# Kernel optimization log

Measured on AMD Instinct MI355X. Metric: run time of the kernel, lower is better.

Reference implementation:

```python
import jax, jax.numpy as jnp
import numpy as np
import math

B, S, H, N = 64, 512, 768, 16
C_COMP, C_REL = 5, 3
P = N * (N - 1)
LN_EPS = 1e-5

# ordered pair indices (i, j), i != j, row-major like the torch double loop
_PAIR_I, _PAIR_J = np.nonzero(~np.eye(N, dtype=bool))
_PAIR_I = jnp.asarray(_PAIR_I)
_PAIR_J = jnp.asarray(_PAIR_J)


def setup_inputs() -> dict:
    key = jax.random.key(0)
    ks = jax.random.split(key, 20)
    sc = 0.02
    p = lambda k, shape: (jax.random.normal(k, shape, jnp.float32) * sc)
    return {
        "last_hidden_state": jax.random.normal(ks[0], (B, S, H), jnp.float32),
        "span_starts": jax.random.randint(ks[1], (B, N), 0, 480).astype(jnp.int32),
        "span_lengths": jax.random.randint(ks[2], (B, N), 0, 31).astype(jnp.int32),
        "components": jax.random.randint(ks[3], (B, N), 0, C_COMP).astype(jnp.int32),
        "relations": jax.random.randint(ks[4], (B, P), 0, C_REL).astype(jnp.int32),
        # comp_classifier: Linear(H,512) -> Tanh -> Linear(512,C_COMP)
        "comp_w1": p(ks[5], (H, 512)), "comp_b1": jnp.zeros((512,), jnp.float32),
        "comp_w2": p(ks[6], (512, C_COMP)), "comp_b2": jnp.zeros((C_COMP,), jnp.float32),
        # Attention(H, H), no bias
        "wq": p(ks[7], (H, H)), "wk": p(ks[8], (H, H)), "wv": p(ks[9], (H, H)),
        # LayerNorm(H)
        "ln_g": jnp.ones((H,), jnp.float32), "ln_b": jnp.zeros((H,), jnp.float32),
        # rel_classifier: Linear(2H,512) -> Tanh -> Linear(512,C_REL)
        "rel_w1": p(ks[10], (2 * H, 512)), "rel_b1": jnp.zeros((512,), jnp.float32),
        "rel_w2": p(ks[11], (512, C_REL)), "rel_b2": jnp.zeros((C_REL,), jnp.float32),
    }


def _ce_mean(logits, gold):
    # logits [M, C], gold [M] -> scalar mean cross entropy
    logp = jax.nn.log_softmax(logits, axis=-1)
    return -jnp.mean(jnp.take_along_axis(logp, gold[:, None].astype(jnp.int32), axis=-1))


def reference(last_hidden_state, span_starts, span_lengths, components, relations,
              comp_w1, comp_b1, comp_w2, comp_b2,
              wq, wk, wv, ln_g, ln_b,
              rel_w1, rel_b1, rel_w2, rel_b2):
    # --- per-span mean pooling (inclusive end = start + length), masked+vectorized ---
    pos = jnp.arange(S)
    ends = span_starts + span_lengths
    mask = ((pos[None, None, :] >= span_starts[:, :, None]) &
            (pos[None, None, :] <= ends[:, :, None])).astype(jnp.float32)  # [B,N,S]
    lens = (span_lengths + 1).astype(jnp.float32)
    pooled = jnp.einsum('bns,bsh->bnh', mask, last_hidden_state) / lens[:, :, None]  # [B,N,H]
    # dropout(p=0.2) is identity in eval mode

    # --- component classifier ---
    comp_logits = jnp.tanh(pooled @ comp_w1 + comp_b1) @ comp_w2 + comp_b2  # [B,N,C_COMP]

    # --- small self-attention over spans ---
    q = pooled @ wq; k = pooled @ wk; v = pooled @ wv
    scores = jax.nn.softmax(jnp.einsum('bnd,bmd->bnm', q, k) / math.sqrt(H), axis=-1)
    attn = jnp.einsum('bnm,bmh->bnh', scores, v)

    # --- residual + layernorm ---
    x = pooled + attn
    mu = jnp.mean(x, axis=-1, keepdims=True)
    var = jnp.mean((x - mu) ** 2, axis=-1, keepdims=True)
    x = (x - mu) * jax.lax.rsqrt(var + LN_EPS) * ln_g + ln_b  # [B,N,H]

    # --- O(N^2) pairwise relation classification (ordered pairs i != j) ---
    pair_feat = jnp.concatenate([x[:, _PAIR_I, :], x[:, _PAIR_J, :]], axis=-1)  # [B,P,2H]
    rel_logits = jnp.tanh(pair_feat @ rel_w1 + rel_b1) @ rel_w2 + rel_b2  # [B,P,C_REL]

    loss_comp = _ce_mean(comp_logits.reshape(-1, C_COMP), components.reshape(-1))
    loss_rel = _ce_mean(rel_logits.reshape(-1, C_REL), relations.reshape(-1))
    return (comp_logits.reshape(-1, C_COMP), rel_logits.reshape(-1, C_REL), loss_comp, loss_rel)
```

## Files before the change

### kernel.cpp

```cpp
#include <hip/hip_runtime.h>

#define BB 64
#define SS 512
#define HH 768
#define NSPAN 16
#define PP 240
#define CCOMP 5
#define CREL 3

typedef unsigned short u16;
typedef __attribute__((ext_vector_type(8))) short bf16x8;
typedef __attribute__((ext_vector_type(4))) float f32x4;

__device__ __forceinline__ u16 f2bf(float f) {
    union { float f; unsigned int i; } v; v.f = f;
    unsigned int x = v.i;
    unsigned int lsb = (x >> 16) & 1u;
    x += 0x7fffu + lsb;
    return (u16)(x >> 16);
}

__device__ __forceinline__ float ftanh(float x) {
    float xc = fminf(fmaxf(x, -15.f), 15.f);
    float e = __expf(2.f * xc);
    return (e - 1.f) / (e + 1.f);
}

__global__ __launch_bounds__(256) void prep_kernel(
    const float* __restrict__ cw1, const float* __restrict__ wq,
    const float* __restrict__ wk, const float* __restrict__ wv,
    const float* __restrict__ rw1, u16* __restrict__ wcat_t, u16* __restrict__ relw_t) {
    int blk = blockIdx.x;
    const float* W; int ldw, nt; u16* outp;
    if (blk < 384)        {             W = cw1; ldw = 512; nt = 16; outp = wcat_t; }
    else if (blk < 960)   { blk -= 384; W = wq;  ldw = 768; nt = 24; outp = wcat_t + (size_t)512 * 768; }
    else if (blk < 1536)  { blk -= 960; W = wk;  ldw = 768; nt = 24; outp = wcat_t + (size_t)1280 * 768; }
    else if (blk < 2112)  { blk -= 1536; W = wv; ldw = 768; nt = 24; outp = wcat_t + (size_t)2048 * 768; }
    else if (blk < 2496)  { blk -= 2112; W = rw1; ldw = 512; nt = 16; outp = relw_t; }
    else                  { blk -= 2496; W = rw1 + (size_t)768 * 512; ldw = 512; nt = 16; outp = relw_t + (size_t)512 * 768; }
    int tk = blk / nt, tn = blk % nt;
    int k0 = tk * 32, n0 = tn * 32;
    __shared__ u16 Ls[32][36];
    int tid = threadIdx.x;
    int tx = tid & 31, ty = tid >> 5;
#pragma unroll
    for (int r = 0; r < 4; ++r) {
        int k = ty + r * 8;
        Ls[tx][k] = f2bf(W[(size_t)(k0 + k) * ldw + n0 + tx]);
    }
    __syncthreads();
#pragma unroll
    for (int r = 0; r < 4; ++r) {
        int n = ty + r * 8;
        outp[(size_t)(n0 + n) * 768 + k0 + tx] = Ls[n][tx];
    }
}

__global__ __launch_bounds__(256) void pool_kernel(
    const float* __restrict__ lhs, const int* __restrict__ starts,
    const int* __restrict__ lens, float* __restrict__ pooled, u16* __restrict__ pooled_bf) {
    int bn = blockIdx.x;
    int b = bn >> 4;
    int st = starts[bn];
    int ln = lens[bn];
    int tid = threadIdx.x;
    const float* base = lhs + ((size_t)b * SS + st) * HH;
    float a0 = 0.f, a1 = 0.f, a2 = 0.f;
    for (int s = 0; s <= ln; ++s) {
        const float* row = base + (size_t)s * HH;
        a0 += row[tid];
        a1 += row[tid + 256];
        a2 += row[tid + 512];
    }
    float inv = 1.0f / (float)(ln + 1);
    a0 *= inv; a1 *= inv; a2 *= inv;
    float* out = pooled + (size_t)bn * HH;
    u16* outb = pooled_bf + (size_t)bn * HH;
    out[tid] = a0;       out[tid + 256] = a1;       out[tid + 512] = a2;
    outb[tid] = f2bf(a0); outb[tid + 256] = f2bf(a1); outb[tid + 512] = f2bf(a2);
}

__global__ __launch_bounds__(256) void gemm_pw_kernel(
    const u16* __restrict__ pooled_bf, const u16* __restrict__ wcat_t,
    const float* __restrict__ comp_b1, float* __restrict__ y2) {
    __shared__ u16 As[64][72];
    __shared__ u16 Bs[64][72];
    int ccol0 = blockIdx.x * 64;
    int row0 = blockIdx.y * 64;
    int act = (ccol0 < 512);
    int tid = threadIdx.x;
    int lane = tid & 63, w = tid >> 6;
    int q = lane >> 4, l15 = lane & 15;
    int wm = (w & 1) * 32, wn = (w >> 1) * 32;
    int r = tid >> 2, c0 = (tid & 3) * 16;
    const u16* ga = pooled_bf + (size_t)(row0 + r) * 768 + c0;
    const u16* gb = wcat_t + (size_t)(ccol0 + r) * 768 + c0;
    f32x4 acc[2][2];
#pragma unroll
    for (int i = 0; i < 2; ++i)
#pragma unroll
        for (int j = 0; j < 2; ++j) acc[i][j] = (f32x4){0.f, 0.f, 0.f, 0.f};

    uint4 va0 = *(const uint4*)(ga);
    uint4 va1 = *(const uint4*)(ga + 8);
    uint4 vb0 = *(const uint4*)(gb);
    uint4 vb1 = *(const uint4*)(gb + 8);
    for (int k0 = 0; k0 < 768; k0 += 64) {
        __syncthreads();
        *(uint4*)(&As[r][c0]) = va0;
        *(uint4*)(&As[r][c0 + 8]) = va1;
        *(uint4*)(&Bs[r][c0]) = vb0;
        *(uint4*)(&Bs[r][c0 + 8]) = vb1;
        __syncthreads();
        if (k0 + 64 < 768) {
            va0 = *(const uint4*)(ga + k0 + 64);
            va1 = *(const uint4*)(ga + k0 + 72);
            vb0 = *(const uint4*)(gb + k0 + 64);
            vb1 = *(const uint4*)(gb + k0 + 72);
        }
#pragma unroll
        for (int ks = 0; ks < 2; ++ks) {
            bf16x8 a0 = *(const bf16x8*)(&As[wm + l15][ks * 32 + q * 8]);
            bf16x8 a1 = *(const bf16x8*)(&As[wm + 16 + l15][ks * 32 + q * 8]);
            bf16x8 b0 = *(const bf16x8*)(&Bs[wn + l15][ks * 32 + q * 8]);
            bf16x8 b1 = *(const bf16x8*)(&Bs[wn + 16 + l15][ks * 32 + q * 8]);
            acc[0][0] = __builtin_amdgcn_mfma_f32_16x16x32_bf16(a0, b0, acc[0][0], 0, 0, 0);
            acc[0][1] = __builtin_amdgcn_mfma_f32_16x16x32_bf16(a0, b1, acc[0][1], 0, 0, 0);
            acc[1][0] = __builtin_amdgcn_mfma_f32_16x16x32_bf16(a1, b0, acc[1][0], 0, 0, 0);
            acc[1][1] = __builtin_amdgcn_mfma_f32_16x16x32_bf16(a1, b1, acc[1][1], 0, 0, 0);
        }
    }
#pragma unroll
    for (int tm = 0; tm < 2; ++tm)
#pragma unroll
        for (int tn = 0; tn < 2; ++tn)
#pragma unroll
            for (int reg = 0; reg < 4; ++reg) {
                int rr = row0 + wm + tm * 16 + q * 4 + reg;
                int cc = ccol0 + wn + tn * 16 + l15;
                float v = acc[tm][tn][reg];
                if (act) v = ftanh(v + comp_b1[cc]);
                y2[(size_t)rr * 2816 + cc] = v;
            }
}

__global__ __launch_bounds__(256) void gemm_z_kernel(
    const u16* __restrict__ x_bf, const u16* __restrict__ relw_t, float* __restrict__ Z) {
    __shared__ u16 As[32][72];
    __shared__ u16 Bs[64][72];
    int ccol0 = blockIdx.x * 64;
    int row0 = blockIdx.y * 32;
    int tid = threadIdx.x;
    int lane = tid & 63, w = tid >> 6;
    int q = lane >> 4, l15 = lane & 15;
    int wm = (w & 1) * 16, wn = (w >> 1) * 32;
    int ra = tid >> 3, ca = (tid & 7) * 8;
    int rb = tid >> 2, cb = (tid & 3) * 16;
    const u16* ga = x_bf + (size_t)(row0 + ra) * 768 + ca;
    const u16* gb = relw_t + (size_t)(ccol0 + rb) * 768 + cb;
    f32x4 acc[2];
    acc[0] = (f32x4){0.f, 0.f, 0.f, 0.f};
    acc[1] = (f32x4){0.f, 0.f, 0.f, 0.f};

    uint4 va = *(const uint4*)(ga);
    uint4 vb0 = *(const uint4*)(gb);
    uint4 vb1 = *(const uint4*)(gb + 8);
    for (int k0 = 0; k0 < 768; k0 += 64) {
        __syncthreads();
        *(uint4*)(&As[ra][ca]) = va;
        *(uint4*)(&Bs[rb][cb]) = vb0;
        *(uint4*)(&Bs[rb][cb + 8]) = vb1;
        __syncthreads();
        if (k0 + 64 < 768) {
            va = *(const uint4*)(ga + k0 + 64);
            vb0 = *(const uint4*)(gb + k0 + 64);
            vb1 = *(const uint4*)(gb + k0 + 72);
        }
#pragma unroll
        for (int ks = 0; ks < 2; ++ks) {
            bf16x8 a0 = *(const bf16x8*)(&As[wm + l15][ks * 32 + q * 8]);
            bf16x8 b0 = *(const bf16x8*)(&Bs[wn + l15][ks * 32 + q * 8]);
            bf16x8 b1 = *(const bf16x8*)(&Bs[wn + 16 + l15][ks * 32 + q * 8]);
            acc[0] = __builtin_amdgcn_mfma_f32_16x16x32_bf16(a0, b0, acc[0], 0, 0, 0);
            acc[1] = __builtin_amdgcn_mfma_f32_16x16x32_bf16(a0, b1, acc[1], 0, 0, 0);
        }
    }
#pragma unroll
    for (int tn = 0; tn < 2; ++tn)
#pragma unroll
        for (int reg = 0; reg < 4; ++reg) {
            int rr = row0 + wm + q * 4 + reg;
            int cc = ccol0 + wn + tn * 16 + l15;
            Z[(size_t)rr * 1024 + cc] = acc[tn][reg];
        }
}

__global__ __launch_bounds__(256) void attn_ln_kernel(
    const float* __restrict__ y2, const float* __restrict__ pooled,
    const float* __restrict__ ln_g, const float* __restrict__ ln_b,
    u16* __restrict__ x_bf) {
    __shared__ float ks[16][772];
    __shared__ float Ssm[16][17];
    int b = blockIdx.x;
    int tid = threadIdx.x;
    int n = tid >> 4;
    int hl = tid & 15;

    for (int u = 0; u < 48; ++u) {
        int h = hl + (u << 4);
        ks[n][h] = y2[((size_t)(b * 16 + n)) * 2816 + 1280 + h];
    }
    __syncthreads();

    int m = tid & 15;
    const float* qrow = y2 + ((size_t)(b * 16 + n)) * 2816 + 512;
    float dot = 0.f;
    for (int h = 0; h < 768; h += 4) {
        float4 qv = *(const float4*)(qrow + h);
        float4 kv = *(const float4*)(&ks[m][h]);
        dot += qv.x * kv.x + qv.y * kv.y + qv.z * kv.z + qv.w * kv.w;
    }
    float sval = dot * 0.03608439182435161f;
    float mx = sval;
#pragma unroll
    for (int off = 8; off >= 1; off >>= 1) mx = fmaxf(mx, __shfl_xor(mx, off, 16));
    float pexp = __expf(sval - mx);
    float psum = pexp;
#pragma unroll
    for (int off = 8; off >= 1; off >>= 1) psum += __shfl_xor(psum, off, 16);
    Ssm[n][m] = pexp / psum;
    __syncthreads();

    for (int u = 0; u < 48; ++u) {
        int h = hl + (u << 4);
        ks[n][h] = y2[((size_t)(b * 16 + n)) * 2816 + 2048 + h];
    }
    __syncthreads();

    float sc[16];
#pragma unroll
    for (int mm = 0; mm < 16; ++mm) sc[mm] = Ssm[n][mm];
    int row = b * 16 + n;
    const float* prow = pooled + (size_t)row * HH;
    float xv[48];
    float ssum = 0.f, ssq = 0.f;
    for (int u = 0; u < 48; ++u) {
        int h = hl + (u << 4);
        float a = 0.f;
#pragma unroll
        for (int mm = 0; mm < 16; ++mm) a += sc[mm] * ks[mm][h];
        float v = prow[h] + a;
        xv[u] = v;
        ssum += v;
        ssq += v * v;
    }
#pragma unroll
    for (int off = 8; off >= 1; off >>= 1) {
        ssum += __shfl_xor(ssum, off, 16);
        ssq += __shfl_xor(ssq, off, 16);
    }
    float mu = ssum * (1.0f / 768.0f);
    float var = ssq * (1.0f / 768.0f) - mu * mu;
    float rs = rsqrtf(var + 1e-5f);
    u16* xrow_bf = x_bf + (size_t)row * HH;
    for (int u = 0; u < 48; ++u) {
        int h = hl + (u << 4);
        xrow_bf[h] = f2bf((xv[u] - mu) * rs * ln_g[h] + ln_b[h]);
    }
}

__global__ __launch_bounds__(256) void heads_kernel(
    const float* __restrict__ Z, const float* __restrict__ rb1,
    const float* __restrict__ rw2, const float* __restrict__ rb2,
    const int* __restrict__ rels,
    const float* __restrict__ y2, const float* __restrict__ cw2,
    const float* __restrict__ cb2, const int* __restrict__ comps,
    float* __restrict__ out, float* __restrict__ rel_p, float* __restrict__ comp_p) {
    __shared__ float red[4];
    int wave = threadIdx.x >> 6, lane = threadIdx.x & 63;
    if (blockIdx.x < 3840) {
        int row = blockIdx.x * 4 + wave;
        int b = row / PP;
        int p = row - b * PP;
        int i = p / 15;
        int jj = p - i * 15;
        int j = jj + (jj >= i ? 1 : 0);
        const float* z1 = Z + ((size_t)(b * 16 + i)) * 1024;
        const float* z2 = Z + ((size_t)(b * 16 + j)) * 1024 + 512;
        float a0 = 0.f, a1 = 0.f, a2 = 0.f;
#pragma unroll
        for (int t = 0; t < 8; ++t) {
            int c = lane + (t << 6);
            float h = ftanh(z1[c] + z2[c] + rb1[c]);
            a0 += h * rw2[c * 3 + 0];
            a1 += h * rw2[c * 3 + 1];
            a2 += h * rw2[c * 3 + 2];
        }
#pragma unroll
        for (int off = 32; off >= 1; off >>= 1) {
            a0 += __shfl_down(a0, off);
            a1 += __shfl_down(a1, off);
            a2 += __shfl_down(a2, off);
        }
        if (lane == 0) {
            float l0 = a0 + rb2[0];
            float l1 = a1 + rb2[1];
            float l2 = a2 + rb2[2];
            float mx = fmaxf(l0, fmaxf(l1, l2));
            float se = __expf(l0 - mx) + __expf(l1 - mx) + __expf(l2 - mx);
            float lse = __logf(se) + mx;
            int g = rels[row];
            float lg = (g == 0) ? l0 : ((g == 1) ? l1 : l2);
            red[wave] = lse - lg;
            float* o = out + 5120 + (size_t)row * 3;
            o[0] = l0; o[1] = l1; o[2] = l2;
        }
        __syncthreads();
        if (threadIdx.x == 0) rel_p[blockIdx.x] = red[0] + red[1] + red[2] + red[3];
    } else {
        int row = (blockIdx.x - 3840) * 4 + wave;
        const float* hrow = y2 + (size_t)row * 2816;
        float acc[CCOMP] = {0.f, 0.f, 0.f, 0.f, 0.f};
#pragma unroll
        for (int t = 0; t < 8; ++t) {
            int c = lane + (t << 6);
            float h = hrow[c];
#pragma unroll
            for (int cc = 0; cc < CCOMP; ++cc) acc[cc] += h * cw2[c * CCOMP + cc];
        }
#pragma unroll
        for (int cc = 0; cc < CCOMP; ++cc)
#pragma unroll
            for (int off = 32; off >= 1; off >>= 1) acc[cc] += __shfl_down(acc[cc], off);
        if (lane == 0) {
            float l[CCOMP];
            float mx = -1e30f;
#pragma unroll
            for (int cc = 0; cc < CCOMP; ++cc) { l[cc] = acc[cc] + cb2[cc]; mx = fmaxf(mx, l[cc]); }
            float se = 0.f;
#pragma unroll
            for (int cc = 0; cc < CCOMP; ++cc) se += __expf(l[cc] - mx);
            float lse = __logf(se) + mx;
            red[wave] = lse - l[comps[row]];
#pragma unroll
            for (int cc = 0; cc < CCOMP; ++cc) out[row * CCOMP + cc] = l[cc];
        }
        __syncthreads();
        if (threadIdx.x == 0) comp_p[blockIdx.x - 3840] = red[0] + red[1] + red[2] + red[3];
    }
}

__global__ __launch_bounds__(256) void finalize_kernel(
    const float* __restrict__ comp_p, const float* __restrict__ rel_p,
    float* __restrict__ out) {
    __shared__ float rc[4], rr[4];
    int tid = threadIdx.x;
    int wave = tid >> 6, lane = tid & 63;
    float sc = comp_p[tid];
    float sr = 0.f;
#pragma unroll
    for (int k = 0; k < 15; ++k) sr += rel_p[tid + k * 256];
#pragma unroll
    for (int off = 32; off >= 1; off >>= 1) {
        sc += __shfl_down(sc, off);
        sr += __shfl_down(sr, off);
    }
    if (lane == 0) { rc[wave] = sc; rr[wave] = sr; }
    __syncthreads();
    if (tid == 0) {
        out[51200] = (rc[0] + rc[1] + rc[2] + rc[3]) * (1.0f / 1024.0f);
        out[51201] = (rr[0] + rr[1] + rr[2] + rr[3]) * (1.0f / 15360.0f);
    }
}

extern "C" void kernel_launch(void* const* d_in, const int* in_sizes, int n_in,
                              void* d_out, int out_size, void* d_ws, size_t ws_size,
                              hipStream_t stream) {
    const float* lhs     = (const float*)d_in[0];
    const int* starts    = (const int*)d_in[1];
    const int* lens      = (const int*)d_in[2];
    const int* comps     = (const int*)d_in[3];
    const int* rels      = (const int*)d_in[4];
    const float* comp_w1 = (const float*)d_in[5];
    const float* comp_b1 = (const float*)d_in[6];
    const float* comp_w2 = (const float*)d_in[7];
    const float* comp_b2 = (const float*)d_in[8];
    const float* wq      = (const float*)d_in[9];
    const float* wk      = (const float*)d_in[10];
    const float* wv      = (const float*)d_in[11];
    const float* ln_g    = (const float*)d_in[12];
    const float* ln_b    = (const float*)d_in[13];
    const float* rel_w1  = (const float*)d_in[14];
    const float* rel_b1  = (const float*)d_in[15];
    const float* rel_w2  = (const float*)d_in[16];
    const float* rel_b2  = (const float*)d_in[17];
    float* out = (float*)d_out;
    float* ws = (float*)d_ws;

    float* pooled = ws;
    float* y2     = pooled + 786432;
    float* Z      = y2 + 2883584;
    float* comp_p = Z + 1048576;
    float* rel_p  = comp_p + 256;
    u16* pooled_bf = (u16*)(rel_p + 3840);
    u16* x_bf      = pooled_bf + 786432;
    u16* wcat_t    = x_bf + 786432;
    u16* relw_t    = wcat_t + 2162688;

    prep_kernel<<<2880, 256, 0, stream>>>(comp_w1, wq, wk, wv, rel_w1, wcat_t, relw_t);
    pool_kernel<<<1024, 256, 0, stream>>>(lhs, starts, lens, pooled, pooled_bf);
    gemm_pw_kernel<<<dim3(44, 16), 256, 0, stream>>>(pooled_bf, wcat_t, comp_b1, y2);
    attn_ln_kernel<<<64, 256, 0, stream>>>(y2, pooled, ln_g, ln_b, x_bf);
    gemm_z_kernel<<<dim3(16, 32), 256, 0, stream>>>(x_bf, relw_t, Z);
    heads_kernel<<<4096, 256, 0, stream>>>(Z, rel_b1, rel_w2, rel_b2, rels,
                                           y2, comp_w2, comp_b2, comps,
                                           out, rel_p, comp_p);
    finalize_kernel<<<1, 256, 0, stream>>>(comp_p, rel_p, out);
}
```

Baseline: 241.0 us.

## Fuse pooling with weight prep, double-buffer GEMMs via direct LDS loads, restructure attention

Merges the pooling kernel into the weight-transpose prep kernel, so the two independent jobs share one launch and the pooling loads become float4. Both GEMMs now stage tiles with global_load_lds into double-buffered, XOR-swizzled shared memory, remap blocks so neighbouring blocks share tiles, and move gemm_z to 64x64 tiles. The attention/LayerNorm kernel now gives each (b,n) row its own wave across 256 blocks instead of one block per batch, and the head kernels vectorize their loads. Together these target launch overhead, LDS bank conflicts, load/compute serialization and low occupancy in attention. The cost is more complex indexing and a full vmcnt(0) wait on every GEMM iteration.

```diff
diff --git a/kernel.cpp b/kernel.cpp
--- a/kernel.cpp
+++ b/kernel.cpp
@@ -3,10 +3,8 @@
 #define BB 64
 #define SS 512
 #define HH 768
-#define NSPAN 16
 #define PP 240
 #define CCOMP 5
-#define CREL 3
 
 typedef unsigned short u16;
 typedef __attribute__((ext_vector_type(8))) short bf16x8;
@@ -26,11 +24,39 @@
     return (e - 1.f) / (e + 1.f);
 }
 
-__global__ __launch_bounds__(256) void prep_kernel(
+__device__ __forceinline__ void gl_lds16(const void* g, void* l) {
+    __builtin_amdgcn_global_load_lds(
+        (const __attribute__((address_space(1))) unsigned int*)g,
+        (__attribute__((address_space(3))) unsigned int*)l, 16, 0, 0);
+}
+
+__global__ __launch_bounds__(256) void prep_pool_kernel(
+    const float* __restrict__ lhs, const int* __restrict__ starts,
+    const int* __restrict__ lens, float* __restrict__ pooled, u16* __restrict__ pooled_bf,
     const float* __restrict__ cw1, const float* __restrict__ wq,
     const float* __restrict__ wk, const float* __restrict__ wv,
     const float* __restrict__ rw1, u16* __restrict__ wcat_t, u16* __restrict__ relw_t) {
     int blk = blockIdx.x;
+    int tid = threadIdx.x;
+    if (blk < 1024) {
+        if (tid >= 192) return;
+        int st = starts[blk];
+        int ln = lens[blk];
+        int b = blk >> 4;
+        const float4* base = (const float4*)(lhs + ((size_t)b * SS + st) * HH);
+        float4 a = {0.f, 0.f, 0.f, 0.f};
+        for (int s = 0; s <= ln; ++s) {
+            float4 v = base[s * 192 + tid];
+            a.x += v.x; a.y += v.y; a.z += v.z; a.w += v.w;
+        }
+        float inv = 1.0f / (float)(ln + 1);
+        a.x *= inv; a.y *= inv; a.z *= inv; a.w *= inv;
+        *(float4*)(pooled + (size_t)blk * HH + tid * 4) = a;
+        ushort4 ub = { f2bf(a.x), f2bf(a.y), f2bf(a.z), f2bf(a.w) };
+        *(ushort4*)(pooled_bf + (size_t)blk * HH + tid * 4) = ub;
+        return;
+    }
+    blk -= 1024;
     const float* W; int ldw, nt; u16* outp;
     if (blk < 384)        {             W = cw1; ldw = 512; nt = 16; outp = wcat_t; }
     else if (blk < 960)   { blk -= 384; W = wq;  ldw = 768; nt = 24; outp = wcat_t + (size_t)512 * 768; }
@@ -41,7 +67,6 @@
     int tk = blk / nt, tn = blk % nt;
     int k0 = tk * 32, n0 = tn * 32;
     __shared__ u16 Ls[32][36];
-    int tid = threadIdx.x;
     int tx = tid & 31, ty = tid >> 5;
 #pragma unroll
     for (int r = 0; r < 4; ++r) {
@@ -56,79 +81,69 @@
     }
 }
 
-__global__ __launch_bounds__(256) void pool_kernel(
-    const float* __restrict__ lhs, const int* __restrict__ starts,
-    const int* __restrict__ lens, float* __restrict__ pooled, u16* __restrict__ pooled_bf) {
-    int bn = blockIdx.x;
-    int b = bn >> 4;
-    int st = starts[bn];
-    int ln = lens[bn];
-    int tid = threadIdx.x;
-    const float* base = lhs + ((size_t)b * SS + st) * HH;
-    float a0 = 0.f, a1 = 0.f, a2 = 0.f;
-    for (int s = 0; s <= ln; ++s) {
-        const float* row = base + (size_t)s * HH;
-        a0 += row[tid];
-        a1 += row[tid + 256];
-        a2 += row[tid + 512];
-    }
-    float inv = 1.0f / (float)(ln + 1);
-    a0 *= inv; a1 *= inv; a2 *= inv;
-    float* out = pooled + (size_t)bn * HH;
-    u16* outb = pooled_bf + (size_t)bn * HH;
-    out[tid] = a0;       out[tid + 256] = a1;       out[tid + 512] = a2;
-    outb[tid] = f2bf(a0); outb[tid + 256] = f2bf(a1); outb[tid + 512] = f2bf(a2);
-}
-
 __global__ __launch_bounds__(256) void gemm_pw_kernel(
     const u16* __restrict__ pooled_bf, const u16* __restrict__ wcat_t,
     const float* __restrict__ comp_b1, float* __restrict__ y2) {
-    __shared__ u16 As[64][72];
-    __shared__ u16 Bs[64][72];
-    int ccol0 = blockIdx.x * 64;
-    int row0 = blockIdx.y * 64;
+    __shared__ u16 As[2][4096];
+    __shared__ u16 Bs[2][4096];
+    int bid = blockIdx.x;
+    int sw = (bid & 7) * 88 + (bid >> 3);
+    int ct = sw >> 4;
+    int rt = sw & 15;
+    int ccol0 = ct * 64, row0 = rt * 64;
     int act = (ccol0 < 512);
     int tid = threadIdx.x;
     int lane = tid & 63, w = tid >> 6;
     int q = lane >> 4, l15 = lane & 15;
     int wm = (w & 1) * 32, wn = (w >> 1) * 32;
-    int r = tid >> 2, c0 = (tid & 3) * 16;
-    const u16* ga = pooled_bf + (size_t)(row0 + r) * 768 + c0;
-    const u16* gb = wcat_t + (size_t)(ccol0 + r) * 768 + c0;
+
+    int srow = w * 8 + (lane >> 3);
+    int sxs = ((lane & 7) * 16) ^ ((srow & 7) << 4);
+    const char* gA0 = (const char*)(pooled_bf + (size_t)(row0 + srow) * 768) + sxs;
+    const char* gA1 = gA0 + (size_t)32 * 768 * 2;
+    const char* gB0 = (const char*)(wcat_t + (size_t)(ccol0 + srow) * 768) + sxs;
+    const char* gB1 = gB0 + (size_t)32 * 768 * 2;
+    char* lA = (char*)As + w * 1024;
+    char* lB = (char*)Bs + w * 1024;
+
     f32x4 acc[2][2];
 #pragma unroll
     for (int i = 0; i < 2; ++i)
 #pragma unroll
         for (int j = 0; j < 2; ++j) acc[i][j] = (f32x4){0.f, 0.f, 0.f, 0.f};
 
-    uint4 va0 = *(const uint4*)(ga);
-    uint4 va1 = *(const uint4*)(ga + 8);
-    uint4 vb0 = *(const uint4*)(gb);
-    uint4 vb1 = *(const uint4*)(gb + 8);
-    for (int k0 = 0; k0 < 768; k0 += 64) {
-        __syncthreads();
-        *(uint4*)(&As[r][c0]) = va0;
-        *(uint4*)(&As[r][c0 + 8]) = va1;
-        *(uint4*)(&Bs[r][c0]) = vb0;
-        *(uint4*)(&Bs[r][c0 + 8]) = vb1;
-        __syncthreads();
-        if (k0 + 64 < 768) {
-            va0 = *(const uint4*)(ga + k0 + 64);
-            va1 = *(const uint4*)(ga + k0 + 72);
-            vb0 = *(const uint4*)(gb + k0 + 64);
-            vb1 = *(const uint4*)(gb + k0 + 72);
-        }
+#define STAGE_PW(BUF, KB) do { \
+        gl_lds16(gA0 + (KB), lA + (BUF) * 8192); \
+        gl_lds16(gA1 + (KB), lA + (BUF) * 8192 + 4096); \
+        gl_lds16(gB0 + (KB), lB + (BUF) * 8192); \
+        gl_lds16(gB1 + (KB), lB + (BUF) * 8192 + 4096); \
+    } while (0)
+
+    STAGE_PW(0, 0);
+    asm volatile("s_waitcnt vmcnt(0)" ::: "memory");
+    __syncthreads();
+    int cur = 0;
+    for (int t = 0; t < 12; ++t) {
+        if (t < 11) STAGE_PW(cur ^ 1, (t + 1) * 128);
+        const char* Ab = (const char*)As + cur * 8192;
+        const char* Bb = (const char*)Bs + cur * 8192;
 #pragma unroll
         for (int ks = 0; ks < 2; ++ks) {
-            bf16x8 a0 = *(const bf16x8*)(&As[wm + l15][ks * 32 + q * 8]);
-            bf16x8 a1 = *(const bf16x8*)(&As[wm + 16 + l15][ks * 32 + q * 8]);
-            bf16x8 b0 = *(const bf16x8*)(&Bs[wn + l15][ks * 32 + q * 8]);
-            bf16x8 b1 = *(const bf16x8*)(&Bs[wn + 16 + l15][ks * 32 + q * 8]);
+            int o = ks * 64 + q * 16;
+            int Ra0 = wm + l15, Ra1 = wm + 16 + l15;
+            int Rb0 = wn + l15, Rb1 = wn + 16 + l15;
+            bf16x8 a0 = *(const bf16x8*)(Ab + Ra0 * 128 + (o ^ ((Ra0 & 7) << 4)));
+            bf16x8 a1 = *(const bf16x8*)(Ab + Ra1 * 128 + (o ^ ((Ra1 & 7) << 4)));
+            bf16x8 b0 = *(const bf16x8*)(Bb + Rb0 * 128 + (o ^ ((Rb0 & 7) << 4)));
+            bf16x8 b1 = *(const bf16x8*)(Bb + Rb1 * 128 + (o ^ ((Rb1 & 7) << 4)));
             acc[0][0] = __builtin_amdgcn_mfma_f32_16x16x32_bf16(a0, b0, acc[0][0], 0, 0, 0);
             acc[0][1] = __builtin_amdgcn_mfma_f32_16x16x32_bf16(a0, b1, acc[0][1], 0, 0, 0);
             acc[1][0] = __builtin_amdgcn_mfma_f32_16x16x32_bf16(a1, b0, acc[1][0], 0, 0, 0);
             acc[1][1] = __builtin_amdgcn_mfma_f32_16x16x32_bf16(a1, b1, acc[1][1], 0, 0, 0);
         }
+        asm volatile("s_waitcnt vmcnt(0)" ::: "memory");
+        __syncthreads();
+        cur ^= 1;
     }
 #pragma unroll
     for (int tm = 0; tm < 2; ++tm)
@@ -146,125 +161,136 @@
 
 __global__ __launch_bounds__(256) void gemm_z_kernel(
     const u16* __restrict__ x_bf, const u16* __restrict__ relw_t, float* __restrict__ Z) {
-    __shared__ u16 As[32][72];
-    __shared__ u16 Bs[64][72];
-    int ccol0 = blockIdx.x * 64;
-    int row0 = blockIdx.y * 32;
+    __shared__ u16 As[2][4096];
+    __shared__ u16 Bs[2][4096];
+    int bid = blockIdx.x;
+    int sw = (bid & 7) * 32 + (bid >> 3);
+    int ct = sw >> 4;
+    int rt = sw & 15;
+    int ccol0 = ct * 64, row0 = rt * 64;
     int tid = threadIdx.x;
     int lane = tid & 63, w = tid >> 6;
     int q = lane >> 4, l15 = lane & 15;
-    int wm = (w & 1) * 16, wn = (w >> 1) * 32;
-    int ra = tid >> 3, ca = (tid & 7) * 8;
-    int rb = tid >> 2, cb = (tid & 3) * 16;
-    const u16* ga = x_bf + (size_t)(row0 + ra) * 768 + ca;
-    const u16* gb = relw_t + (size_t)(ccol0 + rb) * 768 + cb;
-    f32x4 acc[2];
-    acc[0] = (f32x4){0.f, 0.f, 0.f, 0.f};
-    acc[1] = (f32x4){0.f, 0.f, 0.f, 0.f};
-
-    uint4 va = *(const uint4*)(ga);
-    uint4 vb0 = *(const uint4*)(gb);
-    uint4 vb1 = *(const uint4*)(gb + 8);
-    for (int k0 = 0; k0 < 768; k0 += 64) {
+    int wm = (w & 1) * 32, wn = (w >> 1) * 32;
+
+    int srow = w * 8 + (lane >> 3);
+    int sxs = ((lane & 7) * 16) ^ ((srow & 7) << 4);
+    const char* gA0 = (const char*)(x_bf + (size_t)(row0 + srow) * 768) + sxs;
+    const char* gA1 = gA0 + (size_t)32 * 768 * 2;
+    const char* gB0 = (const char*)(relw_t + (size_t)(ccol0 + srow) * 768) + sxs;
+    const char* gB1 = gB0 + (size_t)32 * 768 * 2;
+    char* lA = (char*)As + w * 1024;
+    char* lB = (char*)Bs + w * 1024;
+
+    f32x4 acc[2][2];
+#pragma unroll
+    for (int i = 0; i < 2; ++i)
+#pragma unroll
+        for (int j = 0; j < 2; ++j) acc[i][j] = (f32x4){0.f, 0.f, 0.f, 0.f};
+
+    STAGE_PW(0, 0);
+    asm volatile("s_waitcnt vmcnt(0)" ::: "memory");
+    __syncthreads();
+    int cur = 0;
+    for (int t = 0; t < 12; ++t) {
+        if (t < 11) STAGE_PW(cur ^ 1, (t + 1) * 128);
+        const char* Ab = (const char*)As + cur * 8192;
+        const char* Bb = (const char*)Bs + cur * 8192;
+#pragma unroll
+        for (int ks = 0; ks < 2; ++ks) {
+            int o = ks * 64 + q * 16;
+            int Ra0 = wm + l15, Ra1 = wm + 16 + l15;
+            int Rb0 = wn + l15, Rb1 = wn + 16 + l15;
+            bf16x8 a0 = *(const bf16x8*)(Ab + Ra0 * 128 + (o ^ ((Ra0 & 7) << 4)));
+            bf16x8 a1 = *(const bf16x8*)(Ab + Ra1 * 128 + (o ^ ((Ra1 & 7) << 4)));
+            bf16x8 b0 = *(const bf16x8*)(Bb + Rb0 * 128 + (o ^ ((Rb0 & 7) << 4)));
+            bf16x8 b1 = *(const bf16x8*)(Bb + Rb1 * 128 + (o ^ ((Rb1 & 7) << 4)));
+            acc[0][0] = __builtin_amdgcn_mfma_f32_16x16x32_bf16(a0, b0, acc[0][0], 0, 0, 0);
+            acc[0][1] = __builtin_amdgcn_mfma_f32_16x16x32_bf16(a0, b1, acc[0][1], 0, 0, 0);
+            acc[1][0] = __builtin_amdgcn_mfma_f32_16x16x32_bf16(a1, b0, acc[1][0], 0, 0, 0);
+            acc[1][1] = __builtin_amdgcn_mfma_f32_16x16x32_bf16(a1, b1, acc[1][1], 0, 0, 0);
+        }
+        asm volatile("s_waitcnt vmcnt(0)" ::: "memory");
         __syncthreads();
-        *(uint4*)(&As[ra][ca]) = va;
-        *(uint4*)(&Bs[rb][cb]) = vb0;
-        *(uint4*)(&Bs[rb][cb + 8]) = vb1;
-        __syncthreads();
-        if (k0 + 64 < 768) {
-            va = *(const uint4*)(ga + k0 + 64);
-            vb0 = *(const uint4*)(gb + k0 + 64);
-            vb1 = *(const uint4*)(gb + k0 + 72);
-        }
-#pragma unroll
-        for (int ks = 0; ks < 2; ++ks) {
-            bf16x8 a0 = *(const bf16x8*)(&As[wm + l15][ks * 32 + q * 8]);
-            bf16x8 b0 = *(const bf16x8*)(&Bs[wn + l15][ks * 32 + q * 8]);
-            bf16x8 b1 = *(const bf16x8*)(&Bs[wn + 16 + l15][ks * 32 + q * 8]);
-            acc[0] = __builtin_amdgcn_mfma_f32_16x16x32_bf16(a0, b0, acc[0], 0, 0, 0);
-            acc[1] = __builtin_amdgcn_mfma_f32_16x16x32_bf16(a0, b1, acc[1], 0, 0, 0);
-        }
-    }
-#pragma unroll
-    for (int tn = 0; tn < 2; ++tn)
-#pragma unroll
-        for (int reg = 0; reg < 4; ++reg) {
-            int rr = row0 + wm + q * 4 + reg;
-            int cc = ccol0 + wn + tn * 16 + l15;
-            Z[(size_t)rr * 1024 + cc] = acc[tn][reg];
-        }
+        cur ^= 1;
+    }
+#pragma unroll
+    for (int tm = 0; tm < 2; ++tm)
+#pragma unroll
+        for (int tn = 0; tn < 2; ++tn)
+#pragma unroll
+            for (int reg = 0; reg < 4; ++reg) {
+                int rr = row0 + wm + tm * 16 + q * 4 + reg;
+                int cc = ccol0 + wn + tn * 16 + l15;
+                Z[(size_t)rr * 1024 + cc] = acc[tm][tn][reg];
+            }
 }
 
 __global__ __launch_bounds__(256) void attn_ln_kernel(
     const float* __restrict__ y2, const float* __restrict__ pooled,
     const float* __restrict__ ln_g, const float* __restrict__ ln_b,
     u16* __restrict__ x_bf) {
-    __shared__ float ks[16][772];
-    __shared__ float Ssm[16][17];
-    int b = blockIdx.x;
-    int tid = threadIdx.x;
-    int n = tid >> 4;
-    int hl = tid & 15;
-
-    for (int u = 0; u < 48; ++u) {
-        int h = hl + (u << 4);
-        ks[n][h] = y2[((size_t)(b * 16 + n)) * 2816 + 1280 + h];
-    }
-    __syncthreads();
-
-    int m = tid & 15;
-    const float* qrow = y2 + ((size_t)(b * 16 + n)) * 2816 + 512;
-    float dot = 0.f;
-    for (int h = 0; h < 768; h += 4) {
-        float4 qv = *(const float4*)(qrow + h);
-        float4 kv = *(const float4*)(&ks[m][h]);
-        dot += qv.x * kv.x + qv.y * kv.y + qv.z * kv.z + qv.w * kv.w;
-    }
-    float sval = dot * 0.03608439182435161f;
-    float mx = sval;
-#pragma unroll
-    for (int off = 8; off >= 1; off >>= 1) mx = fmaxf(mx, __shfl_xor(mx, off, 16));
-    float pexp = __expf(sval - mx);
-    float psum = pexp;
-#pragma unroll
-    for (int off = 8; off >= 1; off >>= 1) psum += __shfl_xor(psum, off, 16);
-    Ssm[n][m] = pexp / psum;
-    __syncthreads();
-
-    for (int u = 0; u < 48; ++u) {
-        int h = hl + (u << 4);
-        ks[n][h] = y2[((size_t)(b * 16 + n)) * 2816 + 2048 + h];
-    }
-    __syncthreads();
-
-    float sc[16];
-#pragma unroll
-    for (int mm = 0; mm < 16; ++mm) sc[mm] = Ssm[n][mm];
+    int w = threadIdx.x >> 6, l = threadIdx.x & 63;
+    int gw = blockIdx.x * 4 + w;
+    int b = gw >> 4, n = gw & 15;
+    const float* qrow = y2 + (size_t)(b * 16 + n) * 2816 + 512;
+    float qv[12];
+#pragma unroll
+    for (int u = 0; u < 12; ++u) qv[u] = qrow[l + 64 * u];
+
+    float s[16];
+#pragma unroll
+    for (int m = 0; m < 16; ++m) {
+        const float* krow = y2 + (size_t)(b * 16 + m) * 2816 + 1280;
+        float p = 0.f;
+#pragma unroll
+        for (int u = 0; u < 12; ++u) p += qv[u] * krow[l + 64 * u];
+#pragma unroll
+        for (int off = 32; off >= 1; off >>= 1) p += __shfl_xor(p, off);
+        s[m] = p * 0.03608439182435161f;
+    }
+    float mx = s[0];
+#pragma unroll
+    for (int m = 1; m < 16; ++m) mx = fmaxf(mx, s[m]);
+    float den = 0.f;
+#pragma unroll
+    for (int m = 0; m < 16; ++m) { s[m] = __expf(s[m] - mx); den += s[m]; }
+    float inv = 1.0f / den;
+
+    float acc[12];
+#pragma unroll
+    for (int u = 0; u < 12; ++u) acc[u] = 0.f;
+#pragma unroll
+    for (int m = 0; m < 16; ++m) {
+        const float* vrow = y2 + (size_t)(b * 16 + m) * 2816 + 2048;
+        float pm = s[m] * inv;
+#pragma unroll
+        for (int u = 0; u < 12; ++u) acc[u] += pm * vrow[l + 64 * u];
+    }
+
     int row = b * 16 + n;
     const float* prow = pooled + (size_t)row * HH;
-    float xv[48];
+    float xv[12];
     float ssum = 0.f, ssq = 0.f;
-    for (int u = 0; u < 48; ++u) {
-        int h = hl + (u << 4);
-        float a = 0.f;
-#pragma unroll
-        for (int mm = 0; mm < 16; ++mm) a += sc[mm] * ks[mm][h];
-        float v = prow[h] + a;
+#pragma unroll
+    for (int u = 0; u < 12; ++u) {
+        float v = prow[l + 64 * u] + acc[u];
         xv[u] = v;
         ssum += v;
         ssq += v * v;
     }
 #pragma unroll
-    for (int off = 8; off >= 1; off >>= 1) {
-        ssum += __shfl_xor(ssum, off, 16);
-        ssq += __shfl_xor(ssq, off, 16);
+    for (int off = 32; off >= 1; off >>= 1) {
+        ssum += __shfl_xor(ssum, off);
+        ssq += __shfl_xor(ssq, off);
     }
     float mu = ssum * (1.0f / 768.0f);
     float var = ssq * (1.0f / 768.0f) - mu * mu;
     float rs = rsqrtf(var + 1e-5f);
     u16* xrow_bf = x_bf + (size_t)row * HH;
-    for (int u = 0; u < 48; ++u) {
-        int h = hl + (u << 4);
+#pragma unroll
+    for (int u = 0; u < 12; ++u) {
+        int h = l + 64 * u;
         xrow_bf[h] = f2bf((xv[u] - mu) * rs * ln_g[h] + ln_b[h]);
     }
 }
@@ -289,12 +315,22 @@
         const float* z2 = Z + ((size_t)(b * 16 + j)) * 1024 + 512;
         float a0 = 0.f, a1 = 0.f, a2 = 0.f;
 #pragma unroll
-        for (int t = 0; t < 8; ++t) {
-            int c = lane + (t << 6);
-            float h = ftanh(z1[c] + z2[c] + rb1[c]);
-            a0 += h * rw2[c * 3 + 0];
-            a1 += h * rw2[c * 3 + 1];
-            a2 += h * rw2[c * 3 + 2];
+        for (int t = 0; t < 2; ++t) {
+            int c = (lane + (t << 6)) << 2;
+            float4 zv1 = *(const float4*)(z1 + c);
+            float4 zv2 = *(const float4*)(z2 + c);
+            float4 bv  = *(const float4*)(rb1 + c);
+            float4 w0 = *(const float4*)(rw2 + c * 3);
+            float4 w1 = *(const float4*)(rw2 + c * 3 + 4);
+            float4 w2 = *(const float4*)(rw2 + c * 3 + 8);
+            float fw[12] = {w0.x, w0.y, w0.z, w0.w, w1.x, w1.y, w1.z, w1.w, w2.x, w2.y, w2.z, w2.w};
+            float h0 = ftanh(zv1.x + zv2.x + bv.x);
+            float h1 = ftanh(zv1.y + zv2.y + bv.y);
+            float h2 = ftanh(zv1.z + zv2.z + bv.z);
+            float h3 = ftanh(zv1.w + zv2.w + bv.w);
+            a0 += h0 * fw[0] + h1 * fw[3] + h2 * fw[6] + h3 * fw[9];
+            a1 += h0 * fw[1] + h1 * fw[4] + h2 * fw[7] + h3 * fw[10];
+            a2 += h0 * fw[2] + h1 * fw[5] + h2 * fw[8] + h3 * fw[11];
         }
 #pragma unroll
         for (int off = 32; off >= 1; off >>= 1) {
@@ -306,9 +342,9 @@
             float l0 = a0 + rb2[0];
             float l1 = a1 + rb2[1];
             float l2 = a2 + rb2[2];
-            float mx = fmaxf(l0, fmaxf(l1, l2));
-            float se = __expf(l0 - mx) + __expf(l1 - mx) + __expf(l2 - mx);
-            float lse = __logf(se) + mx;
+            float mxv = fmaxf(l0, fmaxf(l1, l2));
+            float se = __expf(l0 - mxv) + __expf(l1 - mxv) + __expf(l2 - mxv);
+            float lse = __logf(se) + mxv;
             int g = rels[row];
             float lg = (g == 0) ? l0 : ((g == 1) ? l1 : l2);
             red[wave] = lse - lg;
@@ -322,28 +358,39 @@
         const float* hrow = y2 + (size_t)row * 2816;
         float acc[CCOMP] = {0.f, 0.f, 0.f, 0.f, 0.f};
 #pragma unroll
-        for (int t = 0; t < 8; ++t) {
-            int c = lane + (t << 6);
-            float h = hrow[c];
-#pragma unroll
-            for (int cc = 0; cc < CCOMP; ++cc) acc[cc] += h * cw2[c * CCOMP + cc];
+        for (int t = 0; t < 2; ++t) {
+            int c = (lane + (t << 6)) << 2;
+            float4 hv = *(const float4*)(hrow + c);
+            float4 g0 = *(const float4*)(cw2 + c * 5);
+            float4 g1 = *(const float4*)(cw2 + c * 5 + 4);
+            float4 g2 = *(const float4*)(cw2 + c * 5 + 8);
+            float4 g3 = *(const float4*)(cw2 + c * 5 + 12);
+            float4 g4 = *(const float4*)(cw2 + c * 5 + 16);
+            float fw[20] = {g0.x, g0.y, g0.z, g0.w, g1.x, g1.y, g1.z, g1.w,
+                            g2.x, g2.y, g2.z, g2.w, g3.x, g3.y, g3.z, g3.w,
+                            g4.x, g4.y, g4.z, g4.w};
+            float hh[4] = {hv.x, hv.y, hv.z, hv.w};
+#pragma unroll
+            for (int jj = 0; jj < 4; ++jj)
+#pragma unroll
+                for (int cc = 0; cc < CCOMP; ++cc) acc[cc] += hh[jj] * fw[5 * jj + cc];
         }
 #pragma unroll
         for (int cc = 0; cc < CCOMP; ++cc)
 #pragma unroll
             for (int off = 32; off >= 1; off >>= 1) acc[cc] += __shfl_down(acc[cc], off);
         if (lane == 0) {
-            float l[CCOMP];
-            float mx = -1e30f;
-#pragma unroll
-            for (int cc = 0; cc < CCOMP; ++cc) { l[cc] = acc[cc] + cb2[cc]; mx = fmaxf(mx, l[cc]); }
+            float lg[CCOMP];
+            float mxv = -1e30f;
+#pragma unroll
+            for (int cc = 0; cc < CCOMP; ++cc) { lg[cc] = acc[cc] + cb2[cc]; mxv = fmaxf(mxv, lg[cc]); }
             float se = 0.f;
 #pragma unroll
-            for (int cc = 0; cc < CCOMP; ++cc) se += __expf(l[cc] - mx);
-            float lse = __logf(se) + mx;
-            red[wave] = lse - l[comps[row]];
-#pragma unroll
-            for (int cc = 0; cc < CCOMP; ++cc) out[row * CCOMP + cc] = l[cc];
+            for (int cc = 0; cc < CCOMP; ++cc) se += __expf(lg[cc] - mxv);
+            float lse = __logf(se) + mxv;
+            red[wave] = lse - lg[comps[row]];
+#pragma unroll
+            for (int cc = 0; cc < CCOMP; ++cc) out[row * CCOMP + cc] = lg[cc];
         }
         __syncthreads();
         if (threadIdx.x == 0) comp_p[blockIdx.x - 3840] = red[0] + red[1] + red[2] + red[3];
@@ -407,11 +454,11 @@
     u16* wcat_t    = x_bf + 786432;
     u16* relw_t    = wcat_t + 2162688;
 
-    prep_kernel<<<2880, 256, 0, stream>>>(comp_w1, wq, wk, wv, rel_w1, wcat_t, relw_t);
-    pool_kernel<<<1024, 256, 0, stream>>>(lhs, starts, lens, pooled, pooled_bf);
-    gemm_pw_kernel<<<dim3(44, 16), 256, 0, stream>>>(pooled_bf, wcat_t, comp_b1, y2);
-    attn_ln_kernel<<<64, 256, 0, stream>>>(y2, pooled, ln_g, ln_b, x_bf);
-    gemm_z_kernel<<<dim3(16, 32), 256, 0, stream>>>(x_bf, relw_t, Z);
+    prep_pool_kernel<<<3904, 256, 0, stream>>>(lhs, starts, lens, pooled, pooled_bf,
+                                               comp_w1, wq, wk, wv, rel_w1, wcat_t, relw_t);
+    gemm_pw_kernel<<<704, 256, 0, stream>>>(pooled_bf, wcat_t, comp_b1, y2);
+    attn_ln_kernel<<<256, 256, 0, stream>>>(y2, pooled, ln_g, ln_b, x_bf);
+    gemm_z_kernel<<<256, 256, 0, stream>>>(x_bf, relw_t, Z);
     heads_kernel<<<4096, 256, 0, stream>>>(Z, rel_b1, rel_w2, rel_b2, rels,
                                            y2, comp_w2, comp_b2, comps,
                                            out, rel_p, comp_p);
```

Result: faster. 232.7 us (-3.4%).
